# Kernel optimization log

Measured on AMD Instinct MI355X. Metric: run time of the kernel, lower is better.

## Reference

```python
import jax, jax.numpy as jnp
import numpy as np

NEG_INF = -9e15
ALPHA = 0.2  # LeakyReLU negative slope

N = 4096
NFEAT = 512
NHID = 256
NEMBED = 128
NHEADS = 4
OUT1 = NHID // NHEADS   # 64
OUT2 = NEMBED // NHEADS # 32


def _gat_layer(x, adj_mask, W, a):
    # x: [N, F_in]; adj_mask: [N, N] bool; W: [H, F_in, F_out]; a: [H, 2*F_out]
    Fo = W.shape[-1]
    Wh = jnp.einsum('nf,hfo->hno', x, W)                     # [H, N, Fo]
    a_src = jnp.einsum('hno,ho->hn', Wh, a[:, :Fo])          # [H, N]
    a_dst = jnp.einsum('hno,ho->hn', Wh, a[:, Fo:])          # [H, N]
    e = a_src[:, :, None] + a_dst[:, None, :]                # [H, N, N]
    e = jax.nn.leaky_relu(e, negative_slope=ALPHA)
    e = jnp.where(adj_mask[None, :, :], e, NEG_INF)
    att = jax.nn.softmax(e, axis=-1)                         # [H, N, N]
    h = jnp.einsum('hnm,hmo->hno', att, Wh)                  # [H, N, Fo]
    h = jax.nn.elu(h)                                        # concat=True -> ELU
    # concat heads: [N, H*Fo]
    return jnp.transpose(h, (1, 0, 2)).reshape(x.shape[0], -1)


def setup_inputs() -> dict:
    key = jax.random.key(0)
    k1, k2, k3, k4, k5, k6 = jax.random.split(key, 6)
    x = jax.random.normal(k1, (N, NFEAT), dtype=jnp.float32)
    adj = (jax.random.uniform(k2, (N, N)) < 0.01).astype(jnp.float32)
    # per-head GAT params, xavier-uniform-like init (stacked over heads)
    def xavier(k, shape, fan):
        bound = np.sqrt(6.0 / fan)
        return jax.random.uniform(k, shape, minval=-bound, maxval=bound, dtype=jnp.float32)
    W1 = xavier(k3, (NHEADS, NFEAT, OUT1), NFEAT + OUT1)
    a1 = xavier(k4, (NHEADS, 2 * OUT1), 2 * OUT1 + 1)
    W2 = xavier(k5, (NHEADS, NHID, OUT2), NHID + OUT2)
    a2 = xavier(k6, (NHEADS, 2 * OUT2), 2 * OUT2 + 1)
    return {'x': x, 'adj': adj, 'W1': W1, 'a1': a1, 'W2': W2, 'a2': a2}


def reference(x, adj, W1, a1, W2, a2):
    # eval mode: dropout is identity
    adj_mask = adj > 0
    h1 = _gat_layer(x, adj_mask, W1, a1)    # [N, NHID]
    h2 = _gat_layer(h1, adj_mask, W2, a2)   # [N, NEMBED]
    return h2
```

## Files before the change

### kernel.cpp

```cpp
#include <hip/hip_runtime.h>
#include <hip/hip_bf16.h>
#include <cstdint>
#include <cstddef>

#define NNODES 4096
#define NHEADS 4
#define NBR_STRIDE 128

typedef __attribute__((ext_vector_type(8))) short bf16x8v;
typedef __attribute__((ext_vector_type(4))) float f32x4;

__device__ inline unsigned short bf16_rn(float f) {
    unsigned int u = __float_as_uint(f);
    u += 0x7FFFu + ((u >> 16) & 1u);
    return (unsigned short)(u >> 16);
}
__device__ inline float bf16_f32(unsigned short s) {
    return __uint_as_float(((unsigned int)s) << 16);
}

__device__ inline void build_nbr_body(
    const float* __restrict__ adj, int* __restrict__ nbr, int* __restrict__ deg,
    int rowblk) {
    int wave = threadIdx.x >> 6;
    int lane = threadIdx.x & 63;
    int row = rowblk * 4 + wave;
    const float4* arow = reinterpret_cast<const float4*>(adj + (size_t)row * NNODES);
    float4 v[16];
    #pragma unroll
    for (int it = 0; it < 16; ++it) v[it] = arow[it * 64 + lane];
    unsigned long long lt = (1ull << lane) - 1ull;
    int base = 0;
    #pragma unroll
    for (int it = 0; it < 16; ++it) {
        bool b0 = v[it].x > 0.f, b1 = v[it].y > 0.f, b2 = v[it].z > 0.f, b3 = v[it].w > 0.f;
        unsigned long long m0 = __ballot(b0);
        unsigned long long m1 = __ballot(b1);
        unsigned long long m2 = __ballot(b2);
        unsigned long long m3 = __ballot(b3);
        int pre = __popcll(m0 & lt) + __popcll(m1 & lt) +
                  __popcll(m2 & lt) + __popcll(m3 & lt);
        int pos = base + pre;
        int colb = it * 256 + lane * 4;
        if (b0) { if (pos < NBR_STRIDE) nbr[row * NBR_STRIDE + pos] = colb;     pos++; }
        if (b1) { if (pos < NBR_STRIDE) nbr[row * NBR_STRIDE + pos] = colb + 1; pos++; }
        if (b2) { if (pos < NBR_STRIDE) nbr[row * NBR_STRIDE + pos] = colb + 2; pos++; }
        if (b3) { if (pos < NBR_STRIDE) nbr[row * NBR_STRIDE + pos] = colb + 3; pos++; }
        base += __popcll(m0) + __popcll(m1) + __popcll(m2) + __popcll(m3);
    }
    if (lane == 0) deg[row] = base < NBR_STRIDE ? base : NBR_STRIDE;
}

__global__ __launch_bounds__(256) void pack_b_both_kernel(
    const float* __restrict__ W1, const float* __restrict__ W2,
    unsigned short* __restrict__ B1h, unsigned short* __restrict__ B1l,
    unsigned short* __restrict__ B2h, unsigned short* __restrict__ B2l) {
    int t = blockIdx.x * 256 + threadIdx.x;
    if (t < 256 * 512) {
        int n = t >> 9, k = t & 511;
        int h = n >> 6, o = n & 63;
        float v = W1[((size_t)h * 512 + k) * 64 + o];
        unsigned short hi = bf16_rn(v);
        B1h[t] = hi;
        B1l[t] = bf16_rn(v - bf16_f32(hi));
    } else {
        int u = t - 256 * 512;
        if (u < 128 * 256) {
            int n = u >> 8, k = u & 255;
            int h = n >> 5, o = n & 31;
            float v = W2[((size_t)h * 256 + k) * 32 + o];
            unsigned short hi = bf16_rn(v);
            B2h[u] = hi;
            B2l[u] = bf16_rn(v - bf16_f32(hi));
        }
    }
}

template <int K, int N, int FO, int BK, bool ASPLIT>
__device__ inline void gemm_body(
    char* arena,
    const float* __restrict__ A,
    const unsigned short* __restrict__ Ah, const unsigned short* __restrict__ Al,
    const unsigned short* __restrict__ Bh, const unsigned short* __restrict__ Bl,
    const float* __restrict__ a, float* __restrict__ C,
    float* __restrict__ asrc, float* __restrict__ adst,
    int bx, int by) {
    constexpr int BM = 32, BN = 64, LP = BK + 8;
    constexpr int ALD = BM * LP * 2;
    constexpr int BLD = BN * LP * 2;
    typedef unsigned short (*lds_t)[LP];
    lds_t Alh = (lds_t)(arena);
    lds_t All = (lds_t)(arena + ALD);
    lds_t Blh = (lds_t)(arena + 2 * ALD);
    lds_t Bll = (lds_t)(arena + 2 * ALD + BLD);
    float* reds = (float*)(arena + 2 * ALD + 2 * BLD);
    float* redd = (float*)(arena + 2 * ALD + 2 * BLD + 256);
    int tid = threadIdx.x;
    int wave = tid >> 6, lane = tid & 63;
    int rowBase = bx * BM;
    int colBase = by * BN;
    int wr = wave >> 1, wc = wave & 1;
    int lr = lane & 15, lk = lane >> 4;
    f32x4 acc0 = {0.f, 0.f, 0.f, 0.f};
    f32x4 acc1 = {0.f, 0.f, 0.f, 0.f};

    for (int k0 = 0; k0 < K; k0 += BK) {
        if constexpr (BK == 32) {
            int ar = tid >> 3, acf = (tid & 7) * 4;
            int br = tid >> 2, bc = (tid & 3) * 8;
            uint4 bh = *reinterpret_cast<const uint4*>(&Bh[(size_t)(colBase + br) * K + k0 + bc]);
            uint4 bl = *reinterpret_cast<const uint4*>(&Bl[(size_t)(colBase + br) * K + k0 + bc]);
            if constexpr (ASPLIT) {
                uint2 avh = *reinterpret_cast<const uint2*>(&Ah[(size_t)(rowBase + ar) * K + k0 + acf]);
                uint2 avl = *reinterpret_cast<const uint2*>(&Al[(size_t)(rowBase + ar) * K + k0 + acf]);
                __syncthreads();
                *reinterpret_cast<uint2*>(&Alh[ar][acf]) = avh;
                *reinterpret_cast<uint2*>(&All[ar][acf]) = avl;
                *reinterpret_cast<uint4*>(&Blh[br][bc]) = bh;
                *reinterpret_cast<uint4*>(&Bll[br][bc]) = bl;
            } else {
                float4 a0 = *reinterpret_cast<const float4*>(&A[(size_t)(rowBase + ar) * K + k0 + acf]);
                __syncthreads();
                ushort4 h4, l4;
                h4.x = bf16_rn(a0.x); l4.x = bf16_rn(a0.x - bf16_f32(h4.x));
                h4.y = bf16_rn(a0.y); l4.y = bf16_rn(a0.y - bf16_f32(h4.y));
                h4.z = bf16_rn(a0.z); l4.z = bf16_rn(a0.z - bf16_f32(h4.z));
                h4.w = bf16_rn(a0.w); l4.w = bf16_rn(a0.w - bf16_f32(h4.w));
                *reinterpret_cast<ushort4*>(&Alh[ar][acf]) = h4;
                *reinterpret_cast<ushort4*>(&All[ar][acf]) = l4;
                *reinterpret_cast<uint4*>(&Blh[br][bc]) = bh;
                *reinterpret_cast<uint4*>(&Bll[br][bc]) = bl;
            }
        } else {
            int ar = tid >> 3, ac = (tid & 7) * 8;
            uint4 bh0 = *reinterpret_cast<const uint4*>(&Bh[(size_t)(colBase + ar) * K + k0 + ac]);
            uint4 bl0 = *reinterpret_cast<const uint4*>(&Bl[(size_t)(colBase + ar) * K + k0 + ac]);
            uint4 bh1 = *reinterpret_cast<const uint4*>(&Bh[(size_t)(colBase + 32 + ar) * K + k0 + ac]);
            uint4 bl1 = *reinterpret_cast<const uint4*>(&Bl[(size_t)(colBase + 32 + ar) * K + k0 + ac]);
            if constexpr (ASPLIT) {
                uint4 avh = *reinterpret_cast<const uint4*>(&Ah[(size_t)(rowBase + ar) * K + k0 + ac]);
                uint4 avl = *reinterpret_cast<const uint4*>(&Al[(size_t)(rowBase + ar) * K + k0 + ac]);
                __syncthreads();
                *reinterpret_cast<uint4*>(&Alh[ar][ac]) = avh;
                *reinterpret_cast<uint4*>(&All[ar][ac]) = avl;
                *reinterpret_cast<uint4*>(&Blh[ar][ac]) = bh0;
                *reinterpret_cast<uint4*>(&Bll[ar][ac]) = bl0;
                *reinterpret_cast<uint4*>(&Blh[32 + ar][ac]) = bh1;
                *reinterpret_cast<uint4*>(&Bll[32 + ar][ac]) = bl1;
            } else {
                float4 a0 = *reinterpret_cast<const float4*>(&A[(size_t)(rowBase + ar) * K + k0 + ac]);
                float4 a1 = *reinterpret_cast<const float4*>(&A[(size_t)(rowBase + ar) * K + k0 + ac + 4]);
                __syncthreads();
                ushort4 h4, l4;
                h4.x = bf16_rn(a0.x); l4.x = bf16_rn(a0.x - bf16_f32(h4.x));
                h4.y = bf16_rn(a0.y); l4.y = bf16_rn(a0.y - bf16_f32(h4.y));
                h4.z = bf16_rn(a0.z); l4.z = bf16_rn(a0.z - bf16_f32(h4.z));
                h4.w = bf16_rn(a0.w); l4.w = bf16_rn(a0.w - bf16_f32(h4.w));
                *reinterpret_cast<ushort4*>(&Alh[ar][ac]) = h4;
                *reinterpret_cast<ushort4*>(&All[ar][ac]) = l4;
                h4.x = bf16_rn(a1.x); l4.x = bf16_rn(a1.x - bf16_f32(h4.x));
                h4.y = bf16_rn(a1.y); l4.y = bf16_rn(a1.y - bf16_f32(h4.y));
                h4.z = bf16_rn(a1.z); l4.z = bf16_rn(a1.z - bf16_f32(h4.z));
                h4.w = bf16_rn(a1.w); l4.w = bf16_rn(a1.w - bf16_f32(h4.w));
                *reinterpret_cast<ushort4*>(&Alh[ar][ac + 4]) = h4;
                *reinterpret_cast<ushort4*>(&All[ar][ac + 4]) = l4;
                *reinterpret_cast<uint4*>(&Blh[ar][ac]) = bh0;
                *reinterpret_cast<uint4*>(&Bll[ar][ac]) = bl0;
                *reinterpret_cast<uint4*>(&Blh[32 + ar][ac]) = bh1;
                *reinterpret_cast<uint4*>(&Bll[32 + ar][ac]) = bl1;
            }
        }
        __syncthreads();
        #pragma unroll
        for (int ks = 0; ks < BK / 32; ++ks) {
            int kb = ks * 32 + lk * 8;
            bf16x8v ah = *reinterpret_cast<const bf16x8v*>(&Alh[wr * 16 + lr][kb]);
            bf16x8v al = *reinterpret_cast<const bf16x8v*>(&All[wr * 16 + lr][kb]);
            bf16x8v b0h = *reinterpret_cast<const bf16x8v*>(&Blh[wc * 32 + lr][kb]);
            bf16x8v b0l = *reinterpret_cast<const bf16x8v*>(&Bll[wc * 32 + lr][kb]);
            bf16x8v b1h = *reinterpret_cast<const bf16x8v*>(&Blh[wc * 32 + 16 + lr][kb]);
            bf16x8v b1l = *reinterpret_cast<const bf16x8v*>(&Bll[wc * 32 + 16 + lr][kb]);
            acc0 = __builtin_amdgcn_mfma_f32_16x16x32_bf16(ah, b0h, acc0, 0, 0, 0);
            acc0 = __builtin_amdgcn_mfma_f32_16x16x32_bf16(ah, b0l, acc0, 0, 0, 0);
            acc0 = __builtin_amdgcn_mfma_f32_16x16x32_bf16(al, b0h, acc0, 0, 0, 0);
            acc1 = __builtin_amdgcn_mfma_f32_16x16x32_bf16(ah, b1h, acc1, 0, 0, 0);
            acc1 = __builtin_amdgcn_mfma_f32_16x16x32_bf16(ah, b1l, acc1, 0, 0, 0);
            acc1 = __builtin_amdgcn_mfma_f32_16x16x32_bf16(al, b1h, acc1, 0, 0, 0);
        }
    }
    int crow = rowBase + wr * 16 + lk * 4;
    int ccol = colBase + wc * 32 + lr;
    #pragma unroll
    for (int r = 0; r < 4; ++r) {
        C[(size_t)(crow + r) * N + ccol]      = acc0[r];
        C[(size_t)(crow + r) * N + ccol + 16] = acc1[r];
    }
    int n0 = colBase + wc * 32 + lr;
    int hh = n0 / FO;
    int o0 = n0 % FO;
    int o1 = o0 + 16;
    const float* av = a + hh * 2 * FO;
    float aS0 = av[o0], aS1 = av[o1];
    float aD0 = av[FO + o0], aD1 = av[FO + o1];
    float sv[4], dv[4];
    #pragma unroll
    for (int r = 0; r < 4; ++r) {
        sv[r] = acc0[r] * aS0 + acc1[r] * aS1;
        dv[r] = acc0[r] * aD0 + acc1[r] * aD1;
        #pragma unroll
        for (int msk = 1; msk < 16; msk <<= 1) {
            sv[r] += __shfl_xor(sv[r], msk);
            dv[r] += __shfl_xor(dv[r], msk);
        }
    }
    if constexpr (FO == 64) {
        if (lr == 0) {
            #pragma unroll
            for (int r = 0; r < 4; ++r) {
                reds[wc * 32 + wr * 16 + lk * 4 + r] = sv[r];
                redd[wc * 32 + wr * 16 + lk * 4 + r] = dv[r];
            }
        }
        __syncthreads();
        if (tid < BM) {
            int row = tid;
            asrc[(size_t)(rowBase + row) * NHEADS + by] = reds[row] + reds[32 + row];
            adst[(size_t)(rowBase + row) * NHEADS + by] = redd[row] + redd[32 + row];
        }
    } else {
        if (lr == 0) {
            #pragma unroll
            for (int r = 0; r < 4; ++r) {
                int row = rowBase + wr * 16 + lk * 4 + r;
                asrc[(size_t)row * NHEADS + hh] = sv[r];
                adst[(size_t)row * NHEADS + hh] = dv[r];
            }
        }
    }
}

__global__ __launch_bounds__(256) void fused1_kernel(
    const float* __restrict__ adj, int* __restrict__ nbr, int* __restrict__ deg,
    const float* __restrict__ x,
    const unsigned short* __restrict__ B1h, const unsigned short* __restrict__ B1l,
    const float* __restrict__ a1, float* __restrict__ Wh1,
    float* __restrict__ as1, float* __restrict__ ad1) {
    __shared__ __align__(16) char arena[15872];
    int b = blockIdx.x;
    if (b < 512) {
        gemm_body<512, 256, 64, 32, false>(arena, x, nullptr, nullptr,
                                           B1h, B1l, a1, Wh1, as1, ad1,
                                           b & 127, b >> 7);
    } else {
        build_nbr_body(adj, nbr, deg, b - 512);
    }
}

__global__ __launch_bounds__(256) void gemm2_kernel(
    const unsigned short* __restrict__ Ah, const unsigned short* __restrict__ Al,
    const unsigned short* __restrict__ Bh, const unsigned short* __restrict__ Bl,
    const float* __restrict__ a, float* __restrict__ C,
    float* __restrict__ asrc, float* __restrict__ adst) {
    __shared__ __align__(16) char arena[28160];
    gemm_body<256, 128, 32, 64, true>(arena, nullptr, Ah, Al, Bh, Bl,
                                      a, C, asrc, adst, blockIdx.x, blockIdx.y);
}

template <int FO, bool SPLITOUT>
__global__ __launch_bounds__(256) void agg_kernel(
    const float* __restrict__ Wh,
    const float* __restrict__ asrc, const float* __restrict__ adst,
    const int* __restrict__ nbr, const int* __restrict__ deg,
    float* __restrict__ out,
    unsigned short* __restrict__ outh, unsigned short* __restrict__ outl) {
    int wslot = threadIdx.x >> 6;
    int lane = threadIdx.x & 63;
    int n = blockIdx.x;
    int h = wslot;
    int dg = deg[n];
    const int* lst = nbr + n * NBR_STRIDE;
    float my_as = asrc[(size_t)n * NHEADS + h];

    constexpr int STRIDE = NHEADS * FO;
    constexpr int LPR = FO / 4;
    constexpr int NPS = 64 / LPR;
    int sub = lane / LPR;
    int dim4 = (lane % LPR) * 4;
    const float* whp = Wh + h * FO + dim4;

    float m = -1e30f, s = 0.f;
    f32x4 acc = {0.f, 0.f, 0.f, 0.f};

    int k = sub;
    for (; k + NPS < dg; k += 2 * NPS) {
        int cA = lst[k];
        int cB = lst[k + NPS];
        float eA = my_as + adst[(size_t)cA * NHEADS + h];
        float eB = my_as + adst[(size_t)cB * NHEADS + h];
        eA = eA >= 0.f ? eA : 0.2f * eA;
        eB = eB >= 0.f ? eB : 0.2f * eB;
        float4 vA = *reinterpret_cast<const float4*>(&whp[(size_t)cA * STRIDE]);
        float4 vB = *reinterpret_cast<const float4*>(&whp[(size_t)cB * STRIDE]);
        float mn = fmaxf(m, fmaxf(eA, eB));
        float sc = __expf(m - mn);
        float pA = __expf(eA - mn);
        float pB = __expf(eB - mn);
        s = s * sc + pA + pB;
        acc[0] = acc[0] * sc + pA * vA.x + pB * vB.x;
        acc[1] = acc[1] * sc + pA * vA.y + pB * vB.y;
        acc[2] = acc[2] * sc + pA * vA.z + pB * vB.z;
        acc[3] = acc[3] * sc + pA * vA.w + pB * vB.w;
        m = mn;
    }
    if (k < dg) {
        int c = lst[k];
        float e = my_as + adst[(size_t)c * NHEADS + h];
        e = e >= 0.f ? e : 0.2f * e;
        float4 v = *reinterpret_cast<const float4*>(&whp[(size_t)c * STRIDE]);
        float mn = fmaxf(m, e);
        float sc = __expf(m - mn);
        float p = __expf(e - mn);
        s = s * sc + p;
        acc[0] = acc[0] * sc + p * v.x;
        acc[1] = acc[1] * sc + p * v.y;
        acc[2] = acc[2] * sc + p * v.z;
        acc[3] = acc[3] * sc + p * v.w;
        m = mn;
    }
    #pragma unroll
    for (int off = LPR; off < 64; off <<= 1) {
        float m2 = __shfl_xor(m, off);
        float s2 = __shfl_xor(s, off);
        float a0 = __shfl_xor(acc[0], off);
        float a1 = __shfl_xor(acc[1], off);
        float a2 = __shfl_xor(acc[2], off);
        float a3 = __shfl_xor(acc[3], off);
        float mn = fmaxf(m, m2);
        float sa = __expf(m - mn);
        float sb = __expf(m2 - mn);
        s = s * sa + s2 * sb;
        acc[0] = acc[0] * sa + a0 * sb;
        acc[1] = acc[1] * sa + a1 * sb;
        acc[2] = acc[2] * sa + a2 * sb;
        acc[3] = acc[3] * sa + a3 * sb;
        m = mn;
    }
    if (lane < LPR) {
        float inv = 1.0f / s;
        float r0 = acc[0] * inv;
        float r1 = acc[1] * inv;
        float r2 = acc[2] * inv;
        float r3 = acc[3] * inv;
        r0 = r0 > 0.f ? r0 : expm1f(r0);
        r1 = r1 > 0.f ? r1 : expm1f(r1);
        r2 = r2 > 0.f ? r2 : expm1f(r2);
        r3 = r3 > 0.f ? r3 : expm1f(r3);
        size_t idx = (size_t)n * STRIDE + h * FO + dim4;
        if constexpr (SPLITOUT) {
            ushort4 hv, lv;
            hv.x = bf16_rn(r0); lv.x = bf16_rn(r0 - bf16_f32(hv.x));
            hv.y = bf16_rn(r1); lv.y = bf16_rn(r1 - bf16_f32(hv.y));
            hv.z = bf16_rn(r2); lv.z = bf16_rn(r2 - bf16_f32(hv.z));
            hv.w = bf16_rn(r3); lv.w = bf16_rn(r3 - bf16_f32(hv.w));
            *reinterpret_cast<ushort4*>(&outh[idx]) = hv;
            *reinterpret_cast<ushort4*>(&outl[idx]) = lv;
        } else {
            *reinterpret_cast<float4*>(&out[idx]) = make_float4(r0, r1, r2, r3);
        }
    }
}

extern "C" void kernel_launch(void* const* d_in, const int* in_sizes, int n_in,
                              void* d_out, int out_size, void* d_ws, size_t ws_size,
                              hipStream_t stream) {
    const float* x   = (const float*)d_in[0];
    const float* adj = (const float*)d_in[1];
    const float* W1  = (const float*)d_in[2];
    const float* a1  = (const float*)d_in[3];
    const float* W2  = (const float*)d_in[4];
    const float* a2  = (const float*)d_in[5];
    float* outp = (float*)d_out;

    char* p = (char*)d_ws;
    auto alloc = [&](size_t bytes) -> void* {
        void* r = (void*)p;
        p += (bytes + 255) & ~(size_t)255;
        return r;
    };
    int*   nbr = (int*)alloc((size_t)NNODES * NBR_STRIDE * 4);
    int*   deg = (int*)alloc((size_t)NNODES * 4);
    unsigned short* B1h = (unsigned short*)alloc((size_t)256 * 512 * 2);
    unsigned short* B1l = (unsigned short*)alloc((size_t)256 * 512 * 2);
    unsigned short* B2h = (unsigned short*)alloc((size_t)128 * 256 * 2);
    unsigned short* B2l = (unsigned short*)alloc((size_t)128 * 256 * 2);
    float* Wh1 = (float*)alloc((size_t)NNODES * 256 * 4);
    float* as1 = (float*)alloc((size_t)NHEADS * NNODES * 4);
    float* ad1 = (float*)alloc((size_t)NHEADS * NNODES * 4);
    unsigned short* h1h = (unsigned short*)alloc((size_t)NNODES * 256 * 2);
    unsigned short* h1l = (unsigned short*)alloc((size_t)NNODES * 256 * 2);
    float* Wh2 = (float*)alloc((size_t)NNODES * 128 * 4);
    float* as2 = (float*)alloc((size_t)NHEADS * NNODES * 4);
    float* ad2 = (float*)alloc((size_t)NHEADS * NNODES * 4);

    pack_b_both_kernel<<<dim3((256 * 512 + 128 * 256) / 256), dim3(256), 0, stream>>>(
        W1, W2, B1h, B1l, B2h, B2l);
    fused1_kernel<<<dim3(512 + NNODES / 4), dim3(256), 0, stream>>>(
        adj, nbr, deg, x, B1h, B1l, a1, Wh1, as1, ad1);
    agg_kernel<64, true><<<dim3(NNODES), dim3(256), 0, stream>>>(
        Wh1, as1, ad1, nbr, deg, nullptr, h1h, h1l);
    gemm2_kernel<<<dim3(NNODES / 32, 2), dim3(256), 0, stream>>>(
        h1h, h1l, B2h, B2l, a2, Wh2, as2, ad2);
    agg_kernel<32, false><<<dim3(NNODES), dim3(256), 0, stream>>>(
        Wh2, as2, ad2, nbr, deg, outp, nullptr, nullptr);
}
```

Measured before the change: 64.95 us.

## Two-pass softmax in aggregation, smaller-tile gemm2, reorder fused1 block roles

The aggregation kernel now computes the row max in a first pass, then sums exponentials and weighted features in a second pass unrolled by four. This removes the online-softmax rescaling exps and lets the cross-lane merge become plain additions, at the cost of reading the adst values twice. gemm2 becomes a dedicated kernel with 16-row tiles and one accumulator per wave, doubling its block count for better occupancy. In fused1 the adjacency-scan blocks now come before the GEMM blocks, which may change scheduling overlap.

```diff
diff --git a/kernel.cpp b/kernel.cpp
--- a/kernel.cpp
+++ b/kernel.cpp
@@ -76,16 +76,15 @@
     }
 }
 
-template <int K, int N, int FO, int BK, bool ASPLIT>
-__device__ inline void gemm_body(
+template <int K, int N, int FO>
+__device__ inline void gemm1_body(
     char* arena,
     const float* __restrict__ A,
-    const unsigned short* __restrict__ Ah, const unsigned short* __restrict__ Al,
     const unsigned short* __restrict__ Bh, const unsigned short* __restrict__ Bl,
     const float* __restrict__ a, float* __restrict__ C,
     float* __restrict__ asrc, float* __restrict__ adst,
     int bx, int by) {
-    constexpr int BM = 32, BN = 64, LP = BK + 8;
+    constexpr int BM = 32, BN = 64, BK = 32, LP = BK + 8;
     constexpr int ALD = BM * LP * 2;
     constexpr int BLD = BN * LP * 2;
     typedef unsigned short (*lds_t)[LP];
@@ -105,88 +104,35 @@
     f32x4 acc1 = {0.f, 0.f, 0.f, 0.f};
 
     for (int k0 = 0; k0 < K; k0 += BK) {
-        if constexpr (BK == 32) {
-            int ar = tid >> 3, acf = (tid & 7) * 4;
-            int br = tid >> 2, bc = (tid & 3) * 8;
-            uint4 bh = *reinterpret_cast<const uint4*>(&Bh[(size_t)(colBase + br) * K + k0 + bc]);
-            uint4 bl = *reinterpret_cast<const uint4*>(&Bl[(size_t)(colBase + br) * K + k0 + bc]);
-            if constexpr (ASPLIT) {
-                uint2 avh = *reinterpret_cast<const uint2*>(&Ah[(size_t)(rowBase + ar) * K + k0 + acf]);
-                uint2 avl = *reinterpret_cast<const uint2*>(&Al[(size_t)(rowBase + ar) * K + k0 + acf]);
-                __syncthreads();
-                *reinterpret_cast<uint2*>(&Alh[ar][acf]) = avh;
-                *reinterpret_cast<uint2*>(&All[ar][acf]) = avl;
-                *reinterpret_cast<uint4*>(&Blh[br][bc]) = bh;
-                *reinterpret_cast<uint4*>(&Bll[br][bc]) = bl;
-            } else {
-                float4 a0 = *reinterpret_cast<const float4*>(&A[(size_t)(rowBase + ar) * K + k0 + acf]);
-                __syncthreads();
-                ushort4 h4, l4;
-                h4.x = bf16_rn(a0.x); l4.x = bf16_rn(a0.x - bf16_f32(h4.x));
-                h4.y = bf16_rn(a0.y); l4.y = bf16_rn(a0.y - bf16_f32(h4.y));
-                h4.z = bf16_rn(a0.z); l4.z = bf16_rn(a0.z - bf16_f32(h4.z));
-                h4.w = bf16_rn(a0.w); l4.w = bf16_rn(a0.w - bf16_f32(h4.w));
-                *reinterpret_cast<ushort4*>(&Alh[ar][acf]) = h4;
-                *reinterpret_cast<ushort4*>(&All[ar][acf]) = l4;
-                *reinterpret_cast<uint4*>(&Blh[br][bc]) = bh;
-                *reinterpret_cast<uint4*>(&Bll[br][bc]) = bl;
-            }
-        } else {
-            int ar = tid >> 3, ac = (tid & 7) * 8;
-            uint4 bh0 = *reinterpret_cast<const uint4*>(&Bh[(size_t)(colBase + ar) * K + k0 + ac]);
-            uint4 bl0 = *reinterpret_cast<const uint4*>(&Bl[(size_t)(colBase + ar) * K + k0 + ac]);
-            uint4 bh1 = *reinterpret_cast<const uint4*>(&Bh[(size_t)(colBase + 32 + ar) * K + k0 + ac]);
-            uint4 bl1 = *reinterpret_cast<const uint4*>(&Bl[(size_t)(colBase + 32 + ar) * K + k0 + ac]);
-            if constexpr (ASPLIT) {
-                uint4 avh = *reinterpret_cast<const uint4*>(&Ah[(size_t)(rowBase + ar) * K + k0 + ac]);
-                uint4 avl = *reinterpret_cast<const uint4*>(&Al[(size_t)(rowBase + ar) * K + k0 + ac]);
-                __syncthreads();
-                *reinterpret_cast<uint4*>(&Alh[ar][ac]) = avh;
-                *reinterpret_cast<uint4*>(&All[ar][ac]) = avl;
-                *reinterpret_cast<uint4*>(&Blh[ar][ac]) = bh0;
-                *reinterpret_cast<uint4*>(&Bll[ar][ac]) = bl0;
-                *reinterpret_cast<uint4*>(&Blh[32 + ar][ac]) = bh1;
-                *reinterpret_cast<uint4*>(&Bll[32 + ar][ac]) = bl1;
-            } else {
-                float4 a0 = *reinterpret_cast<const float4*>(&A[(size_t)(rowBase + ar) * K + k0 + ac]);
-                float4 a1 = *reinterpret_cast<const float4*>(&A[(size_t)(rowBase + ar) * K + k0 + ac + 4]);
-                __syncthreads();
-                ushort4 h4, l4;
-                h4.x = bf16_rn(a0.x); l4.x = bf16_rn(a0.x - bf16_f32(h4.x));
-                h4.y = bf16_rn(a0.y); l4.y = bf16_rn(a0.y - bf16_f32(h4.y));
-                h4.z = bf16_rn(a0.z); l4.z = bf16_rn(a0.z - bf16_f32(h4.z));
-                h4.w = bf16_rn(a0.w); l4.w = bf16_rn(a0.w - bf16_f32(h4.w));
-                *reinterpret_cast<ushort4*>(&Alh[ar][ac]) = h4;
-                *reinterpret_cast<ushort4*>(&All[ar][ac]) = l4;
-                h4.x = bf16_rn(a1.x); l4.x = bf16_rn(a1.x - bf16_f32(h4.x));
-                h4.y = bf16_rn(a1.y); l4.y = bf16_rn(a1.y - bf16_f32(h4.y));
-                h4.z = bf16_rn(a1.z); l4.z = bf16_rn(a1.z - bf16_f32(h4.z));
-                h4.w = bf16_rn(a1.w); l4.w = bf16_rn(a1.w - bf16_f32(h4.w));
-                *reinterpret_cast<ushort4*>(&Alh[ar][ac + 4]) = h4;
-                *reinterpret_cast<ushort4*>(&All[ar][ac + 4]) = l4;
-                *reinterpret_cast<uint4*>(&Blh[ar][ac]) = bh0;
-                *reinterpret_cast<uint4*>(&Bll[ar][ac]) = bl0;
-                *reinterpret_cast<uint4*>(&Blh[32 + ar][ac]) = bh1;
-                *reinterpret_cast<uint4*>(&Bll[32 + ar][ac]) = bl1;
-            }
-        }
+        int ar = tid >> 3, acf = (tid & 7) * 4;
+        int br = tid >> 2, bc = (tid & 3) * 8;
+        uint4 bh = *reinterpret_cast<const uint4*>(&Bh[(size_t)(colBase + br) * K + k0 + bc]);
+        uint4 bl = *reinterpret_cast<const uint4*>(&Bl[(size_t)(colBase + br) * K + k0 + bc]);
+        float4 a0 = *reinterpret_cast<const float4*>(&A[(size_t)(rowBase + ar) * K + k0 + acf]);
         __syncthreads();
-        #pragma unroll
-        for (int ks = 0; ks < BK / 32; ++ks) {
-            int kb = ks * 32 + lk * 8;
-            bf16x8v ah = *reinterpret_cast<const bf16x8v*>(&Alh[wr * 16 + lr][kb]);
-            bf16x8v al = *reinterpret_cast<const bf16x8v*>(&All[wr * 16 + lr][kb]);
-            bf16x8v b0h = *reinterpret_cast<const bf16x8v*>(&Blh[wc * 32 + lr][kb]);
-            bf16x8v b0l = *reinterpret_cast<const bf16x8v*>(&Bll[wc * 32 + lr][kb]);
-            bf16x8v b1h = *reinterpret_cast<const bf16x8v*>(&Blh[wc * 32 + 16 + lr][kb]);
-            bf16x8v b1l = *reinterpret_cast<const bf16x8v*>(&Bll[wc * 32 + 16 + lr][kb]);
-            acc0 = __builtin_amdgcn_mfma_f32_16x16x32_bf16(ah, b0h, acc0, 0, 0, 0);
-            acc0 = __builtin_amdgcn_mfma_f32_16x16x32_bf16(ah, b0l, acc0, 0, 0, 0);
-            acc0 = __builtin_amdgcn_mfma_f32_16x16x32_bf16(al, b0h, acc0, 0, 0, 0);
-            acc1 = __builtin_amdgcn_mfma_f32_16x16x32_bf16(ah, b1h, acc1, 0, 0, 0);
-            acc1 = __builtin_amdgcn_mfma_f32_16x16x32_bf16(ah, b1l, acc1, 0, 0, 0);
-            acc1 = __builtin_amdgcn_mfma_f32_16x16x32_bf16(al, b1h, acc1, 0, 0, 0);
-        }
+        ushort4 h4, l4;
+        h4.x = bf16_rn(a0.x); l4.x = bf16_rn(a0.x - bf16_f32(h4.x));
+        h4.y = bf16_rn(a0.y); l4.y = bf16_rn(a0.y - bf16_f32(h4.y));
+        h4.z = bf16_rn(a0.z); l4.z = bf16_rn(a0.z - bf16_f32(h4.z));
+        h4.w = bf16_rn(a0.w); l4.w = bf16_rn(a0.w - bf16_f32(h4.w));
+        *reinterpret_cast<ushort4*>(&Alh[ar][acf]) = h4;
+        *reinterpret_cast<ushort4*>(&All[ar][acf]) = l4;
+        *reinterpret_cast<uint4*>(&Blh[br][bc]) = bh;
+        *reinterpret_cast<uint4*>(&Bll[br][bc]) = bl;
+        __syncthreads();
+        int kb = lk * 8;
+        bf16x8v ah = *reinterpret_cast<const bf16x8v*>(&Alh[wr * 16 + lr][kb]);
+        bf16x8v al = *reinterpret_cast<const bf16x8v*>(&All[wr * 16 + lr][kb]);
+        bf16x8v b0h = *reinterpret_cast<const bf16x8v*>(&Blh[wc * 32 + lr][kb]);
+        bf16x8v b0l = *reinterpret_cast<const bf16x8v*>(&Bll[wc * 32 + lr][kb]);
+        bf16x8v b1h = *reinterpret_cast<const bf16x8v*>(&Blh[wc * 32 + 16 + lr][kb]);
+        bf16x8v b1l = *reinterpret_cast<const bf16x8v*>(&Bll[wc * 32 + 16 + lr][kb]);
+        acc0 = __builtin_amdgcn_mfma_f32_16x16x32_bf16(ah, b0h, acc0, 0, 0, 0);
+        acc0 = __builtin_amdgcn_mfma_f32_16x16x32_bf16(ah, b0l, acc0, 0, 0, 0);
+        acc0 = __builtin_amdgcn_mfma_f32_16x16x32_bf16(al, b0h, acc0, 0, 0, 0);
+        acc1 = __builtin_amdgcn_mfma_f32_16x16x32_bf16(ah, b1h, acc1, 0, 0, 0);
+        acc1 = __builtin_amdgcn_mfma_f32_16x16x32_bf16(ah, b1l, acc1, 0, 0, 0);
+        acc1 = __builtin_amdgcn_mfma_f32_16x16x32_bf16(al, b1h, acc1, 0, 0, 0);
     }
     int crow = rowBase + wr * 16 + lk * 4;
     int ccol = colBase + wc * 32 + lr;
@@ -196,10 +142,9 @@
         C[(size_t)(crow + r) * N + ccol + 16] = acc1[r];
     }
     int n0 = colBase + wc * 32 + lr;
-    int hh = n0 / FO;
     int o0 = n0 % FO;
     int o1 = o0 + 16;
-    const float* av = a + hh * 2 * FO;
+    const float* av = a + by * 2 * FO;
     float aS0 = av[o0], aS1 = av[o1];
     float aD0 = av[FO + o0], aD1 = av[FO + o1];
     float sv[4], dv[4];
@@ -213,29 +158,18 @@
             dv[r] += __shfl_xor(dv[r], msk);
         }
     }
-    if constexpr (FO == 64) {
-        if (lr == 0) {
-            #pragma unroll
-            for (int r = 0; r < 4; ++r) {
-                reds[wc * 32 + wr * 16 + lk * 4 + r] = sv[r];
-                redd[wc * 32 + wr * 16 + lk * 4 + r] = dv[r];
-            }
-        }
-        __syncthreads();
-        if (tid < BM) {
-            int row = tid;
-            asrc[(size_t)(rowBase + row) * NHEADS + by] = reds[row] + reds[32 + row];
-            adst[(size_t)(rowBase + row) * NHEADS + by] = redd[row] + redd[32 + row];
-        }
-    } else {
-        if (lr == 0) {
-            #pragma unroll
-            for (int r = 0; r < 4; ++r) {
-                int row = rowBase + wr * 16 + lk * 4 + r;
-                asrc[(size_t)row * NHEADS + hh] = sv[r];
-                adst[(size_t)row * NHEADS + hh] = dv[r];
-            }
-        }
+    if (lr == 0) {
+        #pragma unroll
+        for (int r = 0; r < 4; ++r) {
+            reds[wc * 32 + wr * 16 + lk * 4 + r] = sv[r];
+            redd[wc * 32 + wr * 16 + lk * 4 + r] = dv[r];
+        }
+    }
+    __syncthreads();
+    if (tid < BM) {
+        int row = tid;
+        asrc[(size_t)(rowBase + row) * NHEADS + by] = reds[row] + reds[32 + row];
+        adst[(size_t)(rowBase + row) * NHEADS + by] = redd[row] + redd[32 + row];
     }
 }
 
@@ -247,12 +181,12 @@
     float* __restrict__ as1, float* __restrict__ ad1) {
     __shared__ __align__(16) char arena[15872];
     int b = blockIdx.x;
-    if (b < 512) {
-        gemm_body<512, 256, 64, 32, false>(arena, x, nullptr, nullptr,
-                                           B1h, B1l, a1, Wh1, as1, ad1,
-                                           b & 127, b >> 7);
+    if (b < NNODES / 4) {
+        build_nbr_body(adj, nbr, deg, b);
     } else {
-        build_nbr_body(adj, nbr, deg, b - 512);
+        int g = b - NNODES / 4;
+        gemm1_body<512, 256, 64>(arena, x, B1h, B1l, a1, Wh1, as1, ad1,
+                                 g & 127, g >> 7);
     }
 }
 
@@ -261,9 +195,81 @@
     const unsigned short* __restrict__ Bh, const unsigned short* __restrict__ Bl,
     const float* __restrict__ a, float* __restrict__ C,
     float* __restrict__ asrc, float* __restrict__ adst) {
-    __shared__ __align__(16) char arena[28160];
-    gemm_body<256, 128, 32, 64, true>(arena, nullptr, Ah, Al, Bh, Bl,
-                                      a, C, asrc, adst, blockIdx.x, blockIdx.y);
+    constexpr int K = 256, N = 128, FO = 32, BM = 16, BK = 64, LP = BK + 8;
+    __shared__ unsigned short Alh[BM][LP], All[BM][LP];
+    __shared__ unsigned short Blh[64][LP], Bll[64][LP];
+    __shared__ float reds[4][16], redd[4][16];
+    int tid = threadIdx.x;
+    int w = tid >> 6, lane = tid & 63;
+    int lr = lane & 15, lk = lane >> 4;
+    int rowBase = blockIdx.x * BM;
+    int colBase = blockIdx.y * 64;
+    f32x4 acc0 = {0.f, 0.f, 0.f, 0.f};
+
+    int ar = tid >> 4, acf = (tid & 15) * 4;
+    int br = tid >> 3, bc = (tid & 7) * 8;
+    for (int k0 = 0; k0 < K; k0 += BK) {
+        uint2 avh = *reinterpret_cast<const uint2*>(&Ah[(size_t)(rowBase + ar) * K + k0 + acf]);
+        uint2 avl = *reinterpret_cast<const uint2*>(&Al[(size_t)(rowBase + ar) * K + k0 + acf]);
+        uint4 bh0 = *reinterpret_cast<const uint4*>(&Bh[(size_t)(colBase + br) * K + k0 + bc]);
+        uint4 bl0 = *reinterpret_cast<const uint4*>(&Bl[(size_t)(colBase + br) * K + k0 + bc]);
+        uint4 bh1 = *reinterpret_cast<const uint4*>(&Bh[(size_t)(colBase + 32 + br) * K + k0 + bc]);
+        uint4 bl1 = *reinterpret_cast<const uint4*>(&Bl[(size_t)(colBase + 32 + br) * K + k0 + bc]);
+        __syncthreads();
+        *reinterpret_cast<uint2*>(&Alh[ar][acf]) = avh;
+        *reinterpret_cast<uint2*>(&All[ar][acf]) = avl;
+        *reinterpret_cast<uint4*>(&Blh[br][bc]) = bh0;
+        *reinterpret_cast<uint4*>(&Bll[br][bc]) = bl0;
+        *reinterpret_cast<uint4*>(&Blh[32 + br][bc]) = bh1;
+        *reinterpret_cast<uint4*>(&Bll[32 + br][bc]) = bl1;
+        __syncthreads();
+        #pragma unroll
+        for (int ks = 0; ks < 2; ++ks) {
+            int kb = ks * 32 + lk * 8;
+            bf16x8v ah = *reinterpret_cast<const bf16x8v*>(&Alh[lr][kb]);
+            bf16x8v al = *reinterpret_cast<const bf16x8v*>(&All[lr][kb]);
+            bf16x8v bhv = *reinterpret_cast<const bf16x8v*>(&Blh[w * 16 + lr][kb]);
+            bf16x8v blv = *reinterpret_cast<const bf16x8v*>(&Bll[w * 16 + lr][kb]);
+            acc0 = __builtin_amdgcn_mfma_f32_16x16x32_bf16(ah, bhv, acc0, 0, 0, 0);
+            acc0 = __builtin_amdgcn_mfma_f32_16x16x32_bf16(ah, blv, acc0, 0, 0, 0);
+            acc0 = __builtin_amdgcn_mfma_f32_16x16x32_bf16(al, bhv, acc0, 0, 0, 0);
+        }
+    }
+    int ccol = colBase + w * 16 + lr;
+    #pragma unroll
+    for (int r = 0; r < 4; ++r)
+        C[(size_t)(rowBase + lk * 4 + r) * N + ccol] = acc0[r];
+    int hh = blockIdx.y * 2 + (w >> 1);
+    int o0 = (w & 1) * 16 + lr;
+    const float* av = a + hh * 2 * FO;
+    float aS0 = av[o0];
+    float aD0 = av[FO + o0];
+    float sv[4], dv[4];
+    #pragma unroll
+    for (int r = 0; r < 4; ++r) {
+        sv[r] = acc0[r] * aS0;
+        dv[r] = acc0[r] * aD0;
+        #pragma unroll
+        for (int msk = 1; msk < 16; msk <<= 1) {
+            sv[r] += __shfl_xor(sv[r], msk);
+            dv[r] += __shfl_xor(dv[r], msk);
+        }
+    }
+    if (lr == 0) {
+        #pragma unroll
+        for (int r = 0; r < 4; ++r) {
+            reds[w][lk * 4 + r] = sv[r];
+            redd[w][lk * 4 + r] = dv[r];
+        }
+    }
+    __syncthreads();
+    if (tid < 32) {
+        int pp = tid >> 4, row = tid & 15;
+        asrc[(size_t)(rowBase + row) * NHEADS + blockIdx.y * 2 + pp] =
+            reds[2 * pp][row] + reds[2 * pp + 1][row];
+        adst[(size_t)(rowBase + row) * NHEADS + blockIdx.y * 2 + pp] =
+            redd[2 * pp][row] + redd[2 * pp + 1][row];
+    }
 }
 
 template <int FO, bool SPLITOUT>
@@ -288,62 +294,72 @@
     int dim4 = (lane % LPR) * 4;
     const float* whp = Wh + h * FO + dim4;
 
-    float m = -1e30f, s = 0.f;
-    f32x4 acc = {0.f, 0.f, 0.f, 0.f};
-
+    float m = -1e30f;
     int k = sub;
-    for (; k + NPS < dg; k += 2 * NPS) {
-        int cA = lst[k];
-        int cB = lst[k + NPS];
+    for (; k + 3 * NPS < dg; k += 4 * NPS) {
+        int cA = lst[k], cB = lst[k + NPS], cC = lst[k + 2 * NPS], cD = lst[k + 3 * NPS];
         float eA = my_as + adst[(size_t)cA * NHEADS + h];
         float eB = my_as + adst[(size_t)cB * NHEADS + h];
+        float eC = my_as + adst[(size_t)cC * NHEADS + h];
+        float eD = my_as + adst[(size_t)cD * NHEADS + h];
         eA = eA >= 0.f ? eA : 0.2f * eA;
         eB = eB >= 0.f ? eB : 0.2f * eB;
+        eC = eC >= 0.f ? eC : 0.2f * eC;
+        eD = eD >= 0.f ? eD : 0.2f * eD;
+        m = fmaxf(m, fmaxf(fmaxf(eA, eB), fmaxf(eC, eD)));
+    }
+    for (; k < dg; k += NPS) {
+        float e = my_as + adst[(size_t)lst[k] * NHEADS + h];
+        e = e >= 0.f ? e : 0.2f * e;
+        m = fmaxf(m, e);
+    }
+    #pragma unroll
+    for (int off = LPR; off < 64; off <<= 1) m = fmaxf(m, __shfl_xor(m, off));
+
+    float s = 0.f;
+    f32x4 acc = {0.f, 0.f, 0.f, 0.f};
+    k = sub;
+    for (; k + 3 * NPS < dg; k += 4 * NPS) {
+        int cA = lst[k], cB = lst[k + NPS], cC = lst[k + 2 * NPS], cD = lst[k + 3 * NPS];
+        float eA = my_as + adst[(size_t)cA * NHEADS + h];
+        float eB = my_as + adst[(size_t)cB * NHEADS + h];
+        float eC = my_as + adst[(size_t)cC * NHEADS + h];
+        float eD = my_as + adst[(size_t)cD * NHEADS + h];
         float4 vA = *reinterpret_cast<const float4*>(&whp[(size_t)cA * STRIDE]);
         float4 vB = *reinterpret_cast<const float4*>(&whp[(size_t)cB * STRIDE]);
-        float mn = fmaxf(m, fmaxf(eA, eB));
-        float sc = __expf(m - mn);
-        float pA = __expf(eA - mn);
-        float pB = __expf(eB - mn);
-        s = s * sc + pA + pB;
-        acc[0] = acc[0] * sc + pA * vA.x + pB * vB.x;
-        acc[1] = acc[1] * sc + pA * vA.y + pB * vB.y;
-        acc[2] = acc[2] * sc + pA * vA.z + pB * vB.z;
-        acc[3] = acc[3] * sc + pA * vA.w + pB * vB.w;
-        m = mn;
-    }
-    if (k < dg) {
+        float4 vC = *reinterpret_cast<const float4*>(&whp[(size_t)cC * STRIDE]);
+        float4 vD = *reinterpret_cast<const float4*>(&whp[(size_t)cD * STRIDE]);
+        eA = eA >= 0.f ? eA : 0.2f * eA;
+        eB = eB >= 0.f ? eB : 0.2f * eB;
+        eC = eC >= 0.f ? eC : 0.2f * eC;
+        eD = eD >= 0.f ? eD : 0.2f * eD;
+        float pA = __expf(eA - m), pB = __expf(eB - m);
+        float pC = __expf(eC - m), pD = __expf(eD - m);
+        s += (pA + pB) + (pC + pD);
+        acc[0] += pA * vA.x + pB * vB.x + pC * vC.x + pD * vD.x;
+        acc[1] += pA * vA.y + pB * vB.y + pC * vC.y + pD * vD.y;
+        acc[2] += pA * vA.z + pB * vB.z + pC * vC.z + pD * vD.z;
+        acc[3] += pA * vA.w + pB * vB.w + pC * vC.w + pD * vD.w;
+    }
+    for (; k < dg; k += NPS) {
         int c = lst[k];
         float e = my_as + adst[(size_t)c * NHEADS + h];
+        float4 v = *reinterpret_cast<const float4*>(&whp[(size_t)c * STRIDE]);
         e = e >= 0.f ? e : 0.2f * e;
-        float4 v = *reinterpret_cast<const float4*>(&whp[(size_t)c * STRIDE]);
-        float mn = fmaxf(m, e);
-        float sc = __expf(m - mn);
-        float p = __expf(e - mn);
-        s = s * sc + p;
-        acc[0] = acc[0] * sc + p * v.x;
-        acc[1] = acc[1] * sc + p * v.y;
-        acc[2] = acc[2] * sc + p * v.z;
-        acc[3] = acc[3] * sc + p * v.w;
-        m = mn;
+        float p = __expf(e - m);
+        s += p;
+        acc[0] += p * v.x;
+        acc[1] += p * v.y;
+        acc[2] += p * v.z;
+        acc[3] += p * v.w;
     }
     #pragma unroll
     for (int off = LPR; off < 64; off <<= 1) {
-        float m2 = __shfl_xor(m, off);
-        float s2 = __shfl_xor(s, off);
-        float a0 = __shfl_xor(acc[0], off);
-        float a1 = __shfl_xor(acc[1], off);
-        float a2 = __shfl_xor(acc[2], off);
-        float a3 = __shfl_xor(acc[3], off);
-        float mn = fmaxf(m, m2);
-        float sa = __expf(m - mn);
-        float sb = __expf(m2 - mn);
-        s = s * sa + s2 * sb;
-        acc[0] = acc[0] * sa + a0 * sb;
-        acc[1] = acc[1] * sa + a1 * sb;
-        acc[2] = acc[2] * sa + a2 * sb;
-        acc[3] = acc[3] * sa + a3 * sb;
-        m = mn;
+        s += __shfl_xor(s, off);
+        acc[0] += __shfl_xor(acc[0], off);
+        acc[1] += __shfl_xor(acc[1], off);
+        acc[2] += __shfl_xor(acc[2], off);
+        acc[3] += __shfl_xor(acc[3], off);
     }
     if (lane < LPR) {
         float inv = 1.0f / s;
@@ -404,11 +420,11 @@
 
     pack_b_both_kernel<<<dim3((256 * 512 + 128 * 256) / 256), dim3(256), 0, stream>>>(
         W1, W2, B1h, B1l, B2h, B2l);
-    fused1_kernel<<<dim3(512 + NNODES / 4), dim3(256), 0, stream>>>(
+    fused1_kernel<<<dim3(NNODES / 4 + 512), dim3(256), 0, stream>>>(
         adj, nbr, deg, x, B1h, B1l, a1, Wh1, as1, ad1);
     agg_kernel<64, true><<<dim3(NNODES), dim3(256), 0, stream>>>(
         Wh1, as1, ad1, nbr, deg, nullptr, h1h, h1l);
-    gemm2_kernel<<<dim3(NNODES / 32, 2), dim3(256), 0, stream>>>(
+    gemm2_kernel<<<dim3(NNODES / 16, 2), dim3(256), 0, stream>>>(
         h1h, h1l, B2h, B2l, a2, Wh2, as2, ad2);
     agg_kernel<32, false><<<dim3(NNODES), dim3(256), 0, stream>>>(
         Wh2, as2, ad2, nbr, deg, outp, nullptr, nullptr);
```

Result: slower. 73.72 us (+13.5%).
